# Kernel tuning notes

Hardware: AMD Instinct MI355X
Metric: run time of the kernel (lower is better)

The kernel has to match this reference:

```python
import jax, jax.numpy as jnp
import numpy as np

B, H1, H2, D, C = 4096, 32, 32, 32, 64


def setup_inputs() -> dict:
    key = jax.random.key(0)
    k1, k2, k3 = jax.random.split(key, 3)
    x = jax.random.normal(k1, (B, H1, D), dtype=jnp.float32)
    y = jax.random.normal(k2, (B, H2, D), dtype=jnp.float32)
    # glorot-uniform-ish kernel of shape (compress_dim, H1, H2)
    limit = float(np.sqrt(6.0 / (H1 + H2)))
    kernel = jax.random.uniform(k3, (C, H1, H2), dtype=jnp.float32,
                                minval=-limit, maxval=limit)
    return {"x": x, "y": y, "kernel": kernel}


def reference(x, y, kernel):
    # Original math: outer[b,i,j,d] = x[b,i,d]*y[b,j,d];
    # output_mat[b,c,d] = sum_{i,j} outer[b,i,j,d] * kernel[c,i,j]
    # Expressed as a fused bilinear contraction (avoids the [B,H1,H2,D] tensor):
    # first fold kernel into y per compress channel, then contract with x.
    t = jnp.einsum('cij,bjd->bcid', kernel, y)       # [B,C,H1,D]
    output_mat = jnp.einsum('bid,bcid->bcd', x, t)   # [B,C,D]
    final_output = jnp.sum(output_mat, axis=-1)      # [B,C]
    return (output_mat, final_output)
```

## Files before the change

kernel.cpp:

```cpp
#include <hip/hip_runtime.h>
#include <hip/hip_fp16.h>


typedef __attribute__((ext_vector_type(8))) _Float16 half8;
typedef __attribute__((ext_vector_type(2))) __fp16 fp16x2;
typedef __attribute__((ext_vector_type(4))) float f32x4;
typedef __attribute__((ext_vector_type(8))) short short8;

__device__ __forceinline__ unsigned int dup_h(float f) {
    union { fp16x2 h; unsigned int u; } w;
    w.h = __builtin_amdgcn_cvt_pkrtz(f, f);
    return w.u;
}
__device__ __forceinline__ fp16x2 pk2(float a, float b) {
    return __builtin_amdgcn_cvt_pkrtz(a, b);
}

__global__ __launch_bounds__(256) void kswz_kernel(const float* __restrict__ kern,
                                                   unsigned short* __restrict__ kswz) {
    int idx  = blockIdx.x * 256 + threadIdx.x;
    int lane = idx & 63;
    int nt   = (idx >> 6) & 3;
    int s    = idx >> 8;
    int c    = nt * 16 + (lane & 15);
    int jb   = (lane >> 4) * 8;
    const float* src = kern + c * 1024 + s * 32 + jb;
    union { half8 h; short8 s8; } v;
#pragma unroll
    for (int t = 0; t < 8; ++t) v.h[t] = (_Float16)src[t];
    *(short8*)(kswz + (size_t)idx * 8) = v.s8;
}

__device__ __forceinline__ void gld_lds16(const void* g, void* l) {
    __builtin_amdgcn_global_load_lds(
        (const __attribute__((address_space(1))) unsigned int*)g,
        (__attribute__((address_space(3))) unsigned int*)l, 16, 0, 0);
}

__global__ __launch_bounds__(256, 2) void cin_main(const float* __restrict__ x,
                                                   const float* __restrict__ y,
                                                   const unsigned short* __restrict__ kswz,
                                                   float* __restrict__ out_mat,
                                                   float* __restrict__ out_fin) {
    __shared__ unsigned int xs[8 * 1024];
    __shared__ __align__(16) unsigned short kb[2][8192];

    const int tid  = threadIdx.x;
    const int wave = tid >> 6;
    const int lane = tid & 63;
    const int quad = lane >> 4;
    const int n16  = lane & 15;
    const int b_blk = blockIdx.x * 8;
    const int cq0   = blockIdx.x & 7;

#pragma unroll
    for (int r = 0; r < 4; ++r)
        gld_lds16(kswz + (size_t)cq0 * 8192 + (r * 256 + tid) * 8,
                  &kb[0][r * 2048 + wave * 512]);

    {
        const float4* xg4 = (const float4*)(x + (size_t)b_blk * 1024);
#pragma unroll
        for (int r = 0; r < 8; ++r) {
            int i4 = r * 256 + tid;
            float4 v = xg4[i4];
            uint4 w;
            w.x = dup_h(v.x); w.y = dup_h(v.y); w.z = dup_h(v.z); w.w = dup_h(v.w);
            *(uint4*)&xs[i4 * 4] = w;
        }
    }

    const int bpair = wave;
    const int b0 = b_blk + bpair * 2;
    fp16x2 yv2[4][4];
#pragma unroll
    for (int mt = 0; mt < 4; ++mt) {
        const int b = b0 + (mt >> 1);
        const int d = n16 + 16 * (mt & 1);
        const float* yp = y + (size_t)b * 1024 + (quad * 8) * 32 + d;
#pragma unroll
        for (int p = 0; p < 4; ++p)
            yv2[mt][p] = pk2(yp[(2 * p) * 32], yp[(2 * p + 1) * 32]);
    }

    f32x4 acc[4][4];
#pragma unroll
    for (int mt = 0; mt < 4; ++mt)
#pragma unroll
        for (int nt = 0; nt < 4; ++nt) acc[mt][nt] = (f32x4){0.f, 0.f, 0.f, 0.f};

    int xoff[4];
#pragma unroll
    for (int mt = 0; mt < 4; ++mt)
        xoff[mt] = (bpair * 2 + (mt >> 1)) * 1024 + n16 + 16 * (mt & 1);

    __syncthreads();

    for (int p8 = 0; p8 < 8; ++p8) {
        if (p8 < 7) {
            const int cn = (cq0 + p8 + 1) & 7;
            unsigned short* dst = &kb[(p8 + 1) & 1][0];
#pragma unroll
            for (int r = 0; r < 4; ++r)
                gld_lds16(kswz + (size_t)cn * 8192 + (r * 256 + tid) * 8,
                          dst + r * 2048 + wave * 512);
        }

        const unsigned short* kbase = &kb[p8 & 1][0];
        const int sb = ((cq0 + p8) & 7) * 4;
#pragma unroll
        for (int k = 0; k < 4; ++k) {
            half8 bf[4];
#pragma unroll
            for (int nt = 0; nt < 4; ++nt)
                bf[nt] = *(const half8*)(kbase + ((k * 4 + nt) * 64 + lane) * 8);
#pragma unroll
            for (int mt = 0; mt < 4; ++mt) {
                union { unsigned int u; fp16x2 h; } xv;
                xv.u = xs[xoff[mt] + (sb + k) * 32];
                union { half8 h8; fp16x2 h2[4]; } af;
#pragma unroll
                for (int p = 0; p < 4; ++p) af.h2[p] = xv.h * yv2[mt][p];
#pragma unroll
                for (int nt = 0; nt < 4; ++nt)
                    acc[mt][nt] = __builtin_amdgcn_mfma_f32_16x16x32_f16(
                        af.h8, bf[nt], acc[mt][nt], 0, 0, 0);
            }
        }
        __syncthreads();
    }

#pragma unroll
    for (int mt = 0; mt < 4; ++mt) {
        const int b = b0 + (mt >> 1);
        const int dbase = 16 * (mt & 1) + quad * 4;
#pragma unroll
        for (int nt = 0; nt < 4; ++nt) {
            const int c = nt * 16 + n16;
            *(f32x4*)(out_mat + (size_t)b * 2048 + c * 32 + dbase) = acc[mt][nt];
        }
    }

#pragma unroll
    for (int a = 0; a < 2; ++a) {
        const int b = b0 + a;
#pragma unroll
        for (int nt = 0; nt < 4; ++nt) {
            float f = 0.f;
#pragma unroll
            for (int t = 0; t < 4; ++t) f += acc[2 * a][nt][t] + acc[2 * a + 1][nt][t];
            f += __shfl_xor(f, 16);
            f += __shfl_xor(f, 32);
            if (lane < 16) out_fin[(size_t)b * 64 + nt * 16 + n16] = f;
        }
    }
}

extern "C" void kernel_launch(void* const* d_in, const int* in_sizes, int n_in,
                              void* d_out, int out_size, void* d_ws, size_t ws_size,
                              hipStream_t stream) {
    const float* x    = (const float*)d_in[0];
    const float* y    = (const float*)d_in[1];
    const float* kern = (const float*)d_in[2];
    float* out_mat = (float*)d_out;
    float* out_fin = (float*)d_out + 4096 * 64 * 32;
    unsigned short* kswz = (unsigned short*)d_ws;

    kswz_kernel<<<32, 256, 0, stream>>>(kern, kswz);
    cin_main<<<512, 256, 0, stream>>>(x, y, kswz, out_mat, out_fin);
}
```

Baseline: 100.8 us.

## Triple-buffer kernel and x chunks via async global-to-LDS loads

```diff
diff --git a/kernel.cpp b/kernel.cpp
--- a/kernel.cpp
+++ b/kernel.cpp
@@ -42,8 +42,8 @@
                                                    const unsigned short* __restrict__ kswz,
                                                    float* __restrict__ out_mat,
                                                    float* __restrict__ out_fin) {
-    __shared__ unsigned int xs[8 * 1024];
-    __shared__ __align__(16) unsigned short kb[2][8192];
+    __shared__ __align__(16) unsigned short kb[3][8192];
+    __shared__ __align__(16) float xb[3][1024];
 
     const int tid  = threadIdx.x;
     const int wave = tid >> 6;
@@ -53,25 +53,23 @@
     const int b_blk = blockIdx.x * 8;
     const int cq0   = blockIdx.x & 7;
 
+    const int xbb = tid >> 5;
+    const int xii = (tid >> 3) & 3;
+    const int xd4 = tid & 7;
+
+    auto issue_chunk = [&](int ci, int slot) {
 #pragma unroll
-    for (int r = 0; r < 4; ++r)
-        gld_lds16(kswz + (size_t)cq0 * 8192 + (r * 256 + tid) * 8,
-                  &kb[0][r * 2048 + wave * 512]);
+        for (int r = 0; r < 4; ++r)
+            gld_lds16(kswz + (size_t)ci * 8192 + (r * 256 + tid) * 8,
+                      &kb[slot][r * 2048 + wave * 512]);
+        gld_lds16(x + (size_t)(b_blk + xbb) * 1024 + ci * 128 + xii * 32 + xd4 * 4,
+                  &xb[slot][wave * 256]);
+    };
 
-    {
-        const float4* xg4 = (const float4*)(x + (size_t)b_blk * 1024);
-#pragma unroll
-        for (int r = 0; r < 8; ++r) {
-            int i4 = r * 256 + tid;
-            float4 v = xg4[i4];
-            uint4 w;
-            w.x = dup_h(v.x); w.y = dup_h(v.y); w.z = dup_h(v.z); w.w = dup_h(v.w);
-            *(uint4*)&xs[i4 * 4] = w;
-        }
-    }
+    issue_chunk(cq0, 0);
+    issue_chunk((cq0 + 1) & 7, 1);
 
-    const int bpair = wave;
-    const int b0 = b_blk + bpair * 2;
+    const int b0 = b_blk + wave * 2;
     fp16x2 yv2[4][4];
 #pragma unroll
     for (int mt = 0; mt < 4; ++mt) {
@@ -89,25 +87,19 @@
 #pragma unroll
         for (int nt = 0; nt < 4; ++nt) acc[mt][nt] = (f32x4){0.f, 0.f, 0.f, 0.f};
 
-    int xoff[4];
 #pragma unroll
-    for (int mt = 0; mt < 4; ++mt)
-        xoff[mt] = (bpair * 2 + (mt >> 1)) * 1024 + n16 + 16 * (mt & 1);
+    for (int p8 = 0; p8 < 8; ++p8) {
+        if (p8 < 7) asm volatile("s_waitcnt vmcnt(5)" ::: "memory");
+        else        asm volatile("s_waitcnt vmcnt(0)" ::: "memory");
+        __builtin_amdgcn_s_barrier();
+        __builtin_amdgcn_sched_barrier(0);
 
-    __syncthreads();
+        if (p8 < 6) issue_chunk((cq0 + p8 + 2) & 7, (p8 + 2) % 3);
 
-    for (int p8 = 0; p8 < 8; ++p8) {
-        if (p8 < 7) {
-            const int cn = (cq0 + p8 + 1) & 7;
-            unsigned short* dst = &kb[(p8 + 1) & 1][0];
-#pragma unroll
-            for (int r = 0; r < 4; ++r)
-                gld_lds16(kswz + (size_t)cn * 8192 + (r * 256 + tid) * 8,
-                          dst + r * 2048 + wave * 512);
-        }
+        const unsigned short* kbase = &kb[p8 % 3][0];
+        const float*          xbase = &xb[p8 % 3][0];
 
-        const unsigned short* kbase = &kb[p8 & 1][0];
-        const int sb = ((cq0 + p8) & 7) * 4;
+        __builtin_amdgcn_s_setprio(1);
 #pragma unroll
         for (int k = 0; k < 4; ++k) {
             half8 bf[4];
@@ -116,8 +108,9 @@
                 bf[nt] = *(const half8*)(kbase + ((k * 4 + nt) * 64 + lane) * 8);
 #pragma unroll
             for (int mt = 0; mt < 4; ++mt) {
+                float xf = xbase[(wave * 2 + (mt >> 1)) * 128 + k * 32 + n16 + 16 * (mt & 1)];
                 union { unsigned int u; fp16x2 h; } xv;
-                xv.u = xs[xoff[mt] + (sb + k) * 32];
+                xv.u = dup_h(xf);
                 union { half8 h8; fp16x2 h2[4]; } af;
 #pragma unroll
                 for (int p = 0; p < 4; ++p) af.h2[p] = xv.h * yv2[mt][p];
@@ -127,7 +120,7 @@
                         af.h8, bf[nt], acc[mt][nt], 0, 0, 0);
             }
         }
-        __syncthreads();
+        __builtin_amdgcn_s_setprio(0);
     }
 
 #pragma unroll
```

Result: no change. 100.7 us, median of 2 (-0.1%).
